# Kernel optimization log

Hardware: AMD Instinct MI355X
Metric: run time of the kernel (lower is better)

## Reference

```python
import jax, jax.numpy as jnp
import numpy as np

H_DIM = 512
FF_DIM = 2048
N_HEAD = 4
N_BLOCK = 3
N_TOKEN = 128
B, S = 8, 1024
LN_EPS = 1e-5


def _layernorm(x, g, b):
    mu = jnp.mean(x, axis=-1, keepdims=True)
    var = jnp.mean(jnp.square(x - mu), axis=-1, keepdims=True)
    return (x - mu) * jax.lax.rsqrt(var + LN_EPS) * g + b


def setup_inputs() -> dict:
    key = jax.random.key(0)
    ks = jax.random.split(key, 20)
    sc = 0.02
    inp = {
        'input_ids': jax.random.randint(ks[0], (B, S), 0, N_TOKEN, dtype=jnp.int32),
        'attention_mask': jnp.ones((B, S), dtype=jnp.int32),
        'emb': jax.random.uniform(ks[1], (N_TOKEN, H_DIM), dtype=jnp.float32),
        'wq': jax.random.normal(ks[2], (N_BLOCK, N_HEAD, H_DIM, H_DIM), dtype=jnp.float32) * sc,
        'wk': jax.random.normal(ks[3], (N_BLOCK, N_HEAD, H_DIM, H_DIM), dtype=jnp.float32) * sc,
        'wv': jax.random.normal(ks[4], (N_BLOCK, N_HEAD, H_DIM, H_DIM), dtype=jnp.float32) * sc,
        'wo_w': jax.random.normal(ks[5], (N_BLOCK, N_HEAD * H_DIM, H_DIM), dtype=jnp.float32) * sc,
        'wo_b': jnp.zeros((N_BLOCK, H_DIM), dtype=jnp.float32),
        'ln1_g': jnp.ones((N_BLOCK, H_DIM), dtype=jnp.float32),
        'ln1_b': jnp.zeros((N_BLOCK, H_DIM), dtype=jnp.float32),
        'ff1_w': jax.random.normal(ks[6], (N_BLOCK, FF_DIM, H_DIM), dtype=jnp.float32) * sc,
        'ff1_b': jnp.zeros((N_BLOCK, FF_DIM), dtype=jnp.float32),
        'ff2_w': jax.random.normal(ks[7], (N_BLOCK, H_DIM, FF_DIM), dtype=jnp.float32) * sc,
        'ff2_b': jnp.zeros((N_BLOCK, H_DIM), dtype=jnp.float32),
        'ln2_g': jnp.ones((N_BLOCK, H_DIM), dtype=jnp.float32),
        'ln2_b': jnp.zeros((N_BLOCK, H_DIM), dtype=jnp.float32),
        'lm_w': jax.random.normal(ks[8], (H_DIM, N_TOKEN), dtype=jnp.float32) * sc,
    }
    return inp


def reference(emb, wq, wk, wv, wo_w, wo_b, ln1_g, ln1_b, ff1_w, ff1_b,
              ff2_w, ff2_b, ln2_g, ln2_b, lm_w, input_ids, attention_mask):
    mask_f = attention_mask.astype(jnp.float32)          # [B,S]
    valid = attention_mask != 0                          # [B,S]

    # Embedding lookup
    x = emb[input_ids]                                   # [B,S,H]

    # Positional encoding: positions assigned sequentially to valid tokens;
    # both even and odd feature slots get the SAME sin value (per source).
    pos = jnp.cumsum(mask_f, axis=-1) - 1.0              # [B,S]
    div = jnp.exp(jnp.arange(0, H_DIM, 2, dtype=jnp.float32) * (-jnp.log(10000.0) / H_DIM))  # [H/2]
    s = jnp.sin(pos[..., None] * div)                    # [B,S,H/2]
    pos_enc = jnp.repeat(s, 2, axis=-1) * mask_f[..., None]
    x = x + pos_enc

    # Allowed attention: causal (key <= query) AND query valid AND key valid
    rows = jnp.arange(S)
    causal = rows[None, :, None] >= rows[None, None, :]  # [1,S,S] (query>=key)
    allowed = causal & valid[:, :, None] & valid[:, None, :]  # [B,S,S]
    neg_inf = jnp.float32(-jnp.inf)
    scale = jnp.sqrt(jnp.float32(H_DIM))

    for l in range(N_BLOCK):
        # Per-head full-width attention (each head uses full H_DIM)
        q = jnp.einsum('bsh,nhd->bnsd', x, wq[l])
        k = jnp.einsum('bsh,nhd->bnsd', x, wk[l])
        v = jnp.einsum('bsh,nhd->bnsd', x, wv[l])
        scores = jnp.einsum('bnsd,bntd->bnst', q, k) / scale      # [B,N,S,S]
        scores = jnp.where(allowed[:, None], scores, neg_inf)
        att = jax.nn.softmax(scores, axis=-1)
        att = jnp.where(jnp.isnan(att), 0.0, att)                  # NaN rows -> 0
        o = jnp.einsum('bnst,bntd->bnsd', att, v)                  # [B,N,S,H]
        o = jnp.transpose(o, (0, 2, 1, 3)).reshape(B, S, N_HEAD * H_DIM)
        mh = o @ wo_w[l] + wo_b[l]
        x = _layernorm(x + mh, ln1_g[l], ln1_b[l])
        # Conv1d with kernel 1 == pointwise linear
        ff = jax.nn.relu(jnp.einsum('bsh,fh->bsf', x, ff1_w[l]) + ff1_b[l])
        ff = jnp.einsum('bsf,hf->bsh', ff, ff2_w[l]) + ff2_b[l]
        x = _layernorm(x + ff, ln2_g[l], ln2_b[l])

    return x @ lm_w                                       # [B,S,N_TOKEN]
```

## Files before the change

kernel.cpp:

```cpp
#include <hip/hip_runtime.h>
#include <hip/hip_bf16.h>

#define S_LEN 1024
#define BATCH 8
#define HD 512
#define FFD 2048
#define NHEAD 4
#define NBLK 3
#define NTOK 128

typedef __bf16 bf16_t;
typedef __bf16 bf16x4_t __attribute__((ext_vector_type(4)));
typedef __bf16 bf16x8_t __attribute__((ext_vector_type(8)));
typedef float f32x4_t __attribute__((ext_vector_type(4)));

typedef __attribute__((address_space(3))) uint32_t lds_u32;
typedef __attribute__((address_space(1))) uint32_t glb_u32;

template<int NI>
__device__ __forceinline__ void ldsread(const bf16_t* __restrict__ buf, int row0,
                                        int fr, int fg, int sw, bf16x8_t (&dst)[NI][2]) {
  #pragma unroll
  for (int i = 0; i < NI; ++i)
    #pragma unroll
    for (int ks = 0; ks < 2; ++ks)
      dst[i][ks] = *(const bf16x8_t*)&buf[(row0 + i*16 + fr)*64 + (((ks*4 + fg) ^ sw) << 3)];
}

template<int IB, int JB>
__device__ __forceinline__ void mquad(f32x4_t (&acc)[8][4],
                                      const bf16x8_t (&af)[4][2], const bf16x8_t (&bf)[2][2]) {
  #pragma unroll
  for (int ks = 0; ks < 2; ++ks)
    #pragma unroll
    for (int i = 0; i < 4; ++i)
      #pragma unroll
      for (int j = 0; j < 2; ++j)
        acc[IB+i][JB+j] = __builtin_amdgcn_mfma_f32_16x16x32_bf16(af[i][ks], bf[j][ks], acc[IB+i][JB+j], 0, 0, 0);
}

template<bool OUT_BF16, bool BIAS, bool RELU, bool TRI, bool CKLIM, bool NORM>
__global__ __launch_bounds__(512, 2)
void gemm256_kernel(const bf16_t* __restrict__ A,
                    const bf16_t* __restrict__ Bt,
                    const float* __restrict__ bias,
                    void* __restrict__ Cv,
                    int M, int N, int K,
                    int lda, int ldb, int ldc,
                    long long sA, long long sB, int bshift, long long sBias,
                    int zshift, long long sC_hi, long long sC_lo,
                    int msub_shift, long long msub_stride,
                    float alpha)
{
  const int zb = blockIdx.z;
  int m0, n0;
  if (TRI) {
    const int idx = blockIdx.x;
    int mi = (int)((sqrtf(8.f * idx + 1.f) - 1.f) * 0.5f);
    while ((mi + 1) * (mi + 2) / 2 <= idx) ++mi;
    while (mi * (mi + 1) / 2 > idx) --mi;
    m0 = mi * 256;
    n0 = (idx - mi * (mi + 1) / 2) * 256;
  } else {
    m0 = blockIdx.x * 256;
    n0 = blockIdx.y * 256;
  }
  int kend = K;
  if (CKLIM) { int ke = m0 + 256; kend = ke < K ? ke : K; }
  const int nt = kend >> 6;

  const bf16_t* Az = A + (long long)zb * sA;
  const bf16_t* Bz = Bt + (long long)(zb >> bshift) * sB;
  const long long coff = ((long long)(zb >> zshift)) * sC_hi
                       + ((long long)(zb & ((1 << zshift) - 1))) * sC_lo;

  __shared__ __align__(16) bf16_t As[2][256 * 64];
  __shared__ __align__(16) bf16_t Bs[2][256 * 64];

  const int tid = threadIdx.x;
  const int lane = tid & 63;
  const int w = tid >> 6;
  const int wm = (w >> 2) * 128;
  const int wn = (w & 3) * 64;
  const int fr = lane & 15;
  const int fg = lane >> 4;
  const int sw = fr & 7;

  const int srow = tid >> 3;
  const int scol8 = tid & 7;
  const int gswz = ((scol8 ^ (srow & 7)) << 3);

  f32x4_t acc[8][4];
  #pragma unroll
  for (int i = 0; i < 8; ++i)
    #pragma unroll
    for (int j = 0; j < 4; ++j)
      acc[i][j] = (f32x4_t){0.f, 0.f, 0.f, 0.f};

  const bf16_t* gA0 = Az + (long long)(m0 + srow) * lda + gswz;
  const bf16_t* gB0 = Bz + (long long)(n0 + srow) * ldb + gswz;

  auto stage_half = [&](int buf, int kt, int h) {
    if (h < 2) {
      const bf16_t* g = gA0 + (long long)(h * 128) * lda + (kt << 6);
      bf16_t* l = &As[buf][(h*128 + srow) * 64 + (scol8 << 3)];
      __builtin_amdgcn_global_load_lds((const glb_u32*)g, (lds_u32*)l, 16, 0, 0);
      __builtin_amdgcn_global_load_lds((const glb_u32*)(g + 64LL*lda), (lds_u32*)(l + 64*64), 16, 0, 0);
    } else {
      const int hh = h - 2;
      const bf16_t* g = gB0 + (long long)(hh * 128) * ldb + (kt << 6);
      bf16_t* l = &Bs[buf][(hh*128 + srow) * 64 + (scol8 << 3)];
      __builtin_amdgcn_global_load_lds((const glb_u32*)g, (lds_u32*)l, 16, 0, 0);
      __builtin_amdgcn_global_load_lds((const glb_u32*)(g + 64LL*ldb), (lds_u32*)(l + 64*64), 16, 0, 0);
    }
  };

  stage_half(0, 0, 0); stage_half(0, 0, 1); stage_half(0, 0, 2); stage_half(0, 0, 3);
  if (nt > 1) { stage_half(1, 1, 0); stage_half(1, 1, 1); }
  if (nt > 1) asm volatile("s_waitcnt vmcnt(4)" ::: "memory");
  else        asm volatile("s_waitcnt vmcnt(0)" ::: "memory");
  __builtin_amdgcn_s_barrier();
  __builtin_amdgcn_sched_barrier(0);

  for (int t = 0; t < nt; ++t) {
    const int cur = t & 1;
    const bf16_t* Ac = &As[cur][0];
    const bf16_t* Bc = &Bs[cur][0];
    bf16x8_t a0[4][2], a1[4][2], b0[2][2], b1[2][2];

    ldsread<4>(Ac, wm, fr, fg, sw, a0);
    ldsread<2>(Bc, wn, fr, fg, sw, b0);
    if (t + 1 < nt) stage_half(cur ^ 1, t + 1, 2);
    mquad<0, 0>(acc, a0, b0);
    ldsread<4>(Ac, wm + 64, fr, fg, sw, a1);
    ldsread<2>(Bc, wn + 32, fr, fg, sw, b1);
    if (t + 1 < nt) stage_half(cur ^ 1, t + 1, 3);
    mquad<4, 2>(acc, a1, b1);

    __builtin_amdgcn_s_barrier();
    __builtin_amdgcn_sched_barrier(0);

    if (t + 2 < nt) stage_half(cur, t + 2, 0);
    mquad<0, 2>(acc, a0, b1);
    if (t + 2 < nt) {
      stage_half(cur, t + 2, 1);
      asm volatile("s_waitcnt vmcnt(4)" ::: "memory");
    } else {
      asm volatile("s_waitcnt vmcnt(0)" ::: "memory");
    }
    mquad<4, 0>(acc, a1, b0);

    __builtin_amdgcn_s_barrier();
    __builtin_amdgcn_sched_barrier(0);
  }

  #pragma unroll
  for (int i = 0; i < 8; ++i) {
    #pragma unroll
    for (int e = 0; e < 4; ++e) {
      const int row = m0 + wm + i*16 + fg*4 + e;
      const long long ro = coff
        + ((long long)(row >> msub_shift)) * msub_stride
        + (long long)(row & ((1 << msub_shift) - 1)) * (long long)ldc;
      float rn = 1.f;
      if (NORM) rn = bias[(long long)zb * sBias + row];
      #pragma unroll
      for (int j = 0; j < 4; ++j) {
        const int col = n0 + wn + j*16 + fr;
        float v = acc[i][j][e] * alpha;
        if (BIAS) v += bias[(long long)zb * sBias + col];
        if (NORM) v *= rn;
        if (RELU) v = v > 0.f ? v : 0.f;
        if (OUT_BF16) ((bf16_t*)Cv)[ro + col] = (bf16_t)v;
        else          ((float*)Cv)[ro + col]  = v;
      }
    }
  }
}

template<bool OUT_BF16, bool BIAS, bool RELU, bool CSKIP, bool CKLIM>
__global__ __launch_bounds__(256, 2)
void gemm_bt_kernel(const bf16_t* __restrict__ A,
                    const bf16_t* __restrict__ Bt,
                    const float* __restrict__ bias,
                    void* __restrict__ Cv,
                    int M, int N, int K,
                    int lda, int ldb, int ldc,
                    long long sA, long long sB, long long sBias,
                    int zshift, long long sC_hi, long long sC_lo,
                    int msub_shift, long long msub_stride,
                    float alpha)
{
  const int zb = blockIdx.z;
  const int m0 = blockIdx.x * 128;
  const int n0 = blockIdx.y * 128;
  if (CSKIP && n0 > m0 + 127) return;
  int kend = K;
  if (CKLIM) { int ke = m0 + 128; kend = ke < K ? ke : K; }

  const bf16_t* Az = A + (long long)zb * sA;
  const bf16_t* Bz = Bt + (long long)zb * sB;
  const long long coff = ((long long)(zb >> zshift)) * sC_hi
                       + ((long long)(zb & ((1 << zshift) - 1))) * sC_lo;

  __shared__ __align__(16) bf16_t As[128 * 64];
  __shared__ __align__(16) bf16_t Bs[128 * 64];

  const int tid = threadIdx.x;
  const int wv = tid >> 6;
  const int lane = tid & 63;
  const int wm = (wv >> 1) * 64;
  const int wn = (wv & 1) * 64;
  const int fr = lane & 15;
  const int fg = lane >> 4;
  const int sw = fr & 7;

  f32x4_t acc[4][4];
  #pragma unroll
  for (int i = 0; i < 4; ++i)
    #pragma unroll
    for (int j = 0; j < 4; ++j)
      acc[i][j] = (f32x4_t){0.f, 0.f, 0.f, 0.f};

  const bf16_t* ga = Az + (long long)(m0 + (wv << 5) + (lane >> 3)) * lda
                   + (((lane & 7) ^ (lane >> 3)) << 3);
  const bf16_t* gb = Bz + (long long)(n0 + (wv << 5) + (lane >> 3)) * ldb
                   + (((lane & 7) ^ (lane >> 3)) << 3);

  for (int k0 = 0; k0 < kend; k0 += 64) {
    #pragma unroll
    for (int s = 0; s < 4; ++s) {
      __builtin_amdgcn_global_load_lds(
        (const glb_u32*)(ga + (long long)s * 8 * lda + k0),
        (lds_u32*)(As + (wv * 4 + s) * 512), 16, 0, 0);
      __builtin_amdgcn_global_load_lds(
        (const glb_u32*)(gb + (long long)s * 8 * ldb + k0),
        (lds_u32*)(Bs + (wv * 4 + s) * 512), 16, 0, 0);
    }
    __syncthreads();
    #pragma unroll
    for (int kc = 0; kc < 2; ++kc) {
      const int ca = ((kc * 4 + fg) ^ sw) << 3;
      bf16x8_t af[4], bfr[4];
      #pragma unroll
      for (int i = 0; i < 4; ++i)
        af[i] = *(const bf16x8_t*)&As[(wm + i*16 + fr) * 64 + ca];
      #pragma unroll
      for (int j = 0; j < 4; ++j)
        bfr[j] = *(const bf16x8_t*)&Bs[(wn + j*16 + fr) * 64 + ca];
      #pragma unroll
      for (int i = 0; i < 4; ++i)
        #pragma unroll
        for (int j = 0; j < 4; ++j)
          acc[i][j] = __builtin_amdgcn_mfma_f32_16x16x32_bf16(af[i], bfr[j], acc[i][j], 0, 0, 0);
    }
    __syncthreads();
  }

  #pragma unroll
  for (int i = 0; i < 4; ++i) {
    #pragma unroll
    for (int e = 0; e < 4; ++e) {
      const int row = m0 + wm + i*16 + fg*4 + e;
      const long long ro = coff
        + ((long long)(row >> msub_shift)) * msub_stride
        + (long long)(row & ((1 << msub_shift) - 1)) * (long long)ldc;
      #pragma unroll
      for (int j = 0; j < 4; ++j) {
        const int col = n0 + wn + j*16 + fr;
        float v = acc[i][j][e] * alpha;
        if (BIAS) v += bias[(long long)zb * sBias + col];
        if (RELU) v = v > 0.f ? v : 0.f;
        if (OUT_BF16) ((bf16_t*)Cv)[ro + col] = (bf16_t)v;
        else          ((float*)Cv)[ro + col]  = v;
      }
    }
  }
}

__global__ void softmax_kernel(bf16_t* __restrict__ scP,
                               const int* __restrict__ mask, int pair0)
{
  const int lane = threadIdx.x & 63;
  const int s = blockIdx.x * 4 + (threadIdx.x >> 6);
  const int pz = blockIdx.y;
  const int b = (pair0 + pz) >> 2;
  bf16_t* row = scP + ((long long)pz * S_LEN + s) * S_LEN;
  const int t0 = lane * 16;

  bf16x8_t r0 = *(const bf16x8_t*)&row[t0];
  bf16x8_t r1 = *(const bf16x8_t*)&row[t0 + 8];
  int4 m4[4];
  #pragma unroll
  for (int q = 0; q < 4; ++q) m4[q] = *(const int4*)&mask[b * S_LEN + t0 + q*4];
  const int* mm = (const int*)m4;

  float v[16]; bool ok[16];
  #pragma unroll
  for (int j = 0; j < 16; ++j) {
    const int t = t0 + j;
    ok[j] = (t <= s) && (mm[j] != 0);
    float raw = (j < 8) ? (float)r0[j] : (float)r1[j - 8];
    v[j] = ok[j] ? raw : -INFINITY;
  }
  float mx = v[0];
  #pragma unroll
  for (int j = 1; j < 16; ++j) mx = fmaxf(mx, v[j]);
  #pragma unroll
  for (int o = 32; o; o >>= 1) mx = fmaxf(mx, __shfl_xor(mx, o));

  float e[16]; float sum = 0.f;
  #pragma unroll
  for (int j = 0; j < 16; ++j) { e[j] = ok[j] ? __expf(v[j] - mx) : 0.f; sum += e[j]; }
  #pragma unroll
  for (int o = 32; o; o >>= 1) sum += __shfl_xor(sum, o);

  const bool qvalid = mask[b * S_LEN + s] != 0;
  const float inv = (qvalid && sum > 0.f) ? 1.f / sum : 0.f;
  bf16x8_t o0, o1;
  #pragma unroll
  for (int j = 0; j < 8; ++j) { o0[j] = (bf16_t)(e[j] * inv); o1[j] = (bf16_t)(e[j+8] * inv); }
  *(bf16x8_t*)&row[t0] = o0;
  *(bf16x8_t*)&row[t0 + 8] = o1;
}

template<typename TIN>
__global__ void transpose_kernel(const TIN* __restrict__ in, bf16_t* __restrict__ out,
                                 int R, int C, long long sIn, long long sOut)
{
  __shared__ float tile[32][33];
  const long long zi = (long long)blockIdx.z * sIn;
  const long long zo = (long long)blockIdx.z * sOut;
  const int c0 = blockIdx.x * 32, r0 = blockIdx.y * 32;
  const int tx = threadIdx.x, ty = threadIdx.y;
  #pragma unroll
  for (int i = 0; i < 4; ++i) {
    int r = r0 + ty + i*8;
    tile[ty + i*8][tx] = (float)in[zi + (long long)r * C + c0 + tx];
  }
  __syncthreads();
  #pragma unroll
  for (int i = 0; i < 4; ++i) {
    int c = c0 + ty + i*8;
    out[zo + (long long)c * R + r0 + tx] = (bf16_t)tile[tx][ty + i*8];
  }
}

__global__ void convert2_kernel(const float* __restrict__ a, const float* __restrict__ b,
                                bf16_t* __restrict__ out, long long n)
{
  long long i = (long long)blockIdx.x * blockDim.x + threadIdx.x;
  long long stride = (long long)gridDim.x * blockDim.x;
  for (; i < 2*n; i += stride)
    out[i] = (bf16_t)(i < n ? a[i] : b[i - n]);
}

__global__ void fill_kernel(float* __restrict__ out, long long n, float v)
{
  long long i = (long long)blockIdx.x * blockDim.x + threadIdx.x;
  long long stride = (long long)gridDim.x * blockDim.x;
  for (; i < n; i += stride) out[i] = v;
}

__global__ void pos_kernel(const int* __restrict__ mask, float* __restrict__ pos)
{
  __shared__ float scn[S_LEN];
  const int b = blockIdx.x, t = threadIdx.x;
  scn[t] = (float)(mask[b * S_LEN + t] != 0);
  __syncthreads();
  for (int off = 1; off < S_LEN; off <<= 1) {
    float add = (t >= off) ? scn[t - off] : 0.f;
    __syncthreads();
    scn[t] += add;
    __syncthreads();
  }
  pos[b * S_LEN + t] = scn[t] - 1.0f;
}

__global__ void embed_kernel(const int* __restrict__ ids, const int* __restrict__ mask,
                             const float* __restrict__ pos, const float* __restrict__ emb,
                             float* __restrict__ x, bf16_t* __restrict__ xb)
{
  const int idx = blockIdx.x * 256 + threadIdx.x;
  const int i = idx & 255;
  const int bs = idx >> 8;
  const int id = ids[bs];
  const float m = (float)(mask[bs] != 0);
  const float p = pos[bs];
  const float dv = __expf(-(float)(2 * i) * (9.210340371976184f / (float)HD));
  const float sv = __sinf(p * dv) * m;
  const float e0 = emb[id * HD + 2*i], e1 = emb[id * HD + 2*i + 1];
  const float x0 = e0 + sv, x1 = e1 + sv;
  x[(long long)bs * HD + 2*i]     = x0;
  x[(long long)bs * HD + 2*i + 1] = x1;
  xb[(long long)bs * HD + 2*i]     = (bf16_t)x0;
  xb[(long long)bs * HD + 2*i + 1] = (bf16_t)x1;
}

__global__ void ln_kernel(float* __restrict__ x, const float* __restrict__ tparts,
                          int ns, long long pstride,
                          const float* __restrict__ bias,
                          const float* __restrict__ g, const float* __restrict__ b,
                          bf16_t* __restrict__ xb)
{
  const int lane = threadIdx.x & 63;
  const long long row = (long long)blockIdx.x * 4 + (threadIdx.x >> 6);
  const int e0 = lane * 8;
  const long long base = row * HD + e0;

  float4 xa = *(const float4*)&x[base];
  float4 xc = *(const float4*)&x[base + 4];
  float4 ba = *(const float4*)&bias[e0];
  float4 bc = *(const float4*)&bias[e0 + 4];
  float v[8] = {xa.x+ba.x, xa.y+ba.y, xa.z+ba.z, xa.w+ba.w,
                xc.x+bc.x, xc.y+bc.y, xc.z+bc.z, xc.w+bc.w};
  for (int i = 0; i < ns; ++i) {
    float4 p0 = *(const float4*)&tparts[i*pstride + base];
    float4 p1 = *(const float4*)&tparts[i*pstride + base + 4];
    v[0]+=p0.x; v[1]+=p0.y; v[2]+=p0.z; v[3]+=p0.w;
    v[4]+=p1.x; v[5]+=p1.y; v[6]+=p1.z; v[7]+=p1.w;
  }
  float s = 0.f;
  #pragma unroll
  for (int j = 0; j < 8; ++j) s += v[j];
  #pragma unroll
  for (int o = 32; o; o >>= 1) s += __shfl_xor(s, o);
  const float mu = s * (1.f / (float)HD);
  float q = 0.f;
  #pragma unroll
  for (int j = 0; j < 8; ++j) { v[j] -= mu; q += v[j]*v[j]; }
  #pragma unroll
  for (int o = 32; o; o >>= 1) q += __shfl_xor(q, o);
  const float inv = rsqrtf(q * (1.f / (float)HD) + 1e-5f);

  float4 ga4 = *(const float4*)&g[e0];
  float4 gc4 = *(const float4*)&g[e0 + 4];
  float4 bb4 = *(const float4*)&b[e0];
  float4 bd4 = *(const float4*)&b[e0 + 4];
  float y[8] = {v[0]*inv*ga4.x+bb4.x, v[1]*inv*ga4.y+bb4.y, v[2]*inv*ga4.z+bb4.z, v[3]*inv*ga4.w+bb4.w,
                v[4]*inv*gc4.x+bd4.x, v[5]*inv*gc4.y+bd4.y, v[6]*inv*gc4.z+bd4.z, v[7]*inv*gc4.w+bd4.w};
  *(float4*)&x[base]     = (float4){y[0],y[1],y[2],y[3]};
  *(float4*)&x[base + 4] = (float4){y[4],y[5],y[6],y[7]};
  bf16x8_t yb;
  #pragma unroll
  for (int j = 0; j < 8; ++j) yb[j] = (bf16_t)y[j];
  *(bf16x8_t*)&xb[base] = yb;
}

extern "C" void kernel_launch(void* const* d_in, const int* in_sizes, int n_in,
                              void* d_out, int out_size, void* d_ws, size_t ws_size,
                              hipStream_t stream)
{
  (void)in_sizes; (void)n_in;
  const int*   ids   = (const int*)d_in[0];
  const int*   amask = (const int*)d_in[1];
  const float* emb   = (const float*)d_in[2];
  const float* wq    = (const float*)d_in[3];
  const float* wk    = (const float*)d_in[4];
  const float* wv    = (const float*)d_in[5];
  const float* wo_w  = (const float*)d_in[6];
  const float* wo_b  = (const float*)d_in[7];
  const float* ln1_g = (const float*)d_in[8];
  const float* ln1_b = (const float*)d_in[9];
  const float* ff1_w = (const float*)d_in[10];
  const float* ff1_b = (const float*)d_in[11];
  const float* ff2_w = (const float*)d_in[12];
  const float* ff2_b = (const float*)d_in[13];
  const float* ln2_g = (const float*)d_in[14];
  const float* ln2_b = (const float*)d_in[15];
  const float* lm_w  = (const float*)d_in[16];

  const long long MROW = (long long)BATCH * S_LEN;
  const size_t MBc = 1ull << 20;
  char* p = (char*)d_ws;
  auto alloc = [&](size_t bytes) { char* r = p; p += (bytes + 255) & ~(size_t)255; return r; };

  float*  x     = (float*) alloc(MROW * HD * 4);
  bf16_t* xb    = (bf16_t*)alloc(MROW * HD * 2);
  bf16_t* ob    = (bf16_t*)alloc(MROW * (NHEAD*HD) * 2);
  bf16_t* wqkb  = (bf16_t*)alloc(8LL * HD * HD * 2);
  bf16_t* wvT   = (bf16_t*)alloc(4LL * HD * HD * 2);
  bf16_t* Gt    = (bf16_t*)alloc(4LL * HD * HD * 2);
  bf16_t* woT   = (bf16_t*)alloc((long long)HD * FFD * 2);
  bf16_t* wff1  = (bf16_t*)alloc((long long)FFD * HD * 2);
  bf16_t* wff2  = (bf16_t*)alloc((long long)HD * FFD * 2);
  bf16_t* lmT   = (bf16_t*)alloc((long long)NTOK * HD * 2);
  float*  pos   = (float*) alloc(MROW * 4);

  const size_t used = (size_t)(p - (char*)d_ws);
  const size_t rem  = ws_size > used ? ws_size - used : 0;

  int P = 0, SK = 2;
  if      (rem >= 128 * MBc) { P = 32; SK = 4; }
  else if (rem >= 64 * MBc)  { P = 8;  SK = 2; }
  if (P == 0) {
    fill_kernel<<<1024, 256, 0, stream>>>((float*)d_out, (long long)out_size,
                                          (float)(ws_size >> 20));
    return;
  }

  char* A = p;
  const long long pairE = (long long)S_LEN * HD;
  bf16_t* qc  = (bf16_t*)A;
  bf16_t* vTc = qc  + (long long)P * pairE;
  bf16_t* scb = vTc + (long long)P * pairE;
  float*  tmp = (float*)A;
  bf16_t* ffb = (bf16_t*)(A + (size_t)SK * 16 * MBc);

  const dim3 tb(32, 8);
  transpose_kernel<float><<<dim3(4,16,1), tb, 0, stream>>>(lm_w, lmT, HD, NTOK, 0, 0);
  pos_kernel<<<BATCH, S_LEN, 0, stream>>>(amask, pos);
  embed_kernel<<<8192, 256, 0, stream>>>(ids, amask, pos, emb, x, xb);

  const int nch = 32 / P;
  const int bpc = P / NHEAD;

  for (int l = 0; l < NBLK; ++l) {
    convert2_kernel<<<2048, 256, 0, stream>>>(
      wq + (long long)l*NHEAD*HD*HD, wk + (long long)l*NHEAD*HD*HD, wqkb, 4LL*HD*HD);
    transpose_kernel<float><<<dim3(16,16,4), tb, 0, stream>>>(
      wv + (long long)l*NHEAD*HD*HD, wvT, HD, HD, (long long)HD*HD, (long long)HD*HD);
    transpose_kernel<float><<<dim3(16,64,1), tb, 0, stream>>>(
      wo_w + (long long)l*FFD*HD, woT, FFD, HD, 0, 0);
    convert2_kernel<<<2048, 256, 0, stream>>>(
      ff1_w + (long long)l*FFD*HD, ff2_w + (long long)l*HD*FFD, wff1, (long long)FFD*HD);
    gemm_bt_kernel<true,false,false,false,false><<<dim3(4,4,4),256,0,stream>>>(
      wqkb + 4LL*HD*HD, wqkb, nullptr, Gt,
      HD, HD, HD, HD, HD, HD,
      (long long)HD*HD, (long long)HD*HD, 0,
      30, 0, (long long)HD*HD,
      30, 0, 1.f);

    for (int c = 0; c < nch; ++c) {
      const int b0 = c * bpc;
      const int pair0 = b0 * NHEAD;
      const int Mch = bpc * S_LEN;

      gemm256_kernel<true,false,false,false,false,false><<<dim3(Mch/256,2,4),512,0,stream>>>(
        xb + (long long)b0*S_LEN*HD, Gt, nullptr, qc, Mch, HD, HD, HD, HD, HD,
        0, (long long)HD*HD, 0, 0,
        2, 0, pairE,
        10, (long long)NHEAD*pairE, 1.f);

      gemm256_kernel<true,false,false,false,false,false><<<dim3(8,4,bpc),512,0,stream>>>(
        wvT, xb + (long long)b0*S_LEN*HD, nullptr, vTc,
        2048, S_LEN, HD, HD, HD, S_LEN,
        0, (long long)S_LEN*HD, 0, 0,
        0, (long long)NHEAD*HD*S_LEN, 0,
        9, (long long)HD*S_LEN, 1.f);

      gemm256_kernel<true,false,false,true,false,false><<<dim3(10,1,P),512,0,stream>>>(
        qc, xb + (long long)b0*S_LEN*HD, nullptr, scb,
        S_LEN, S_LEN, HD, HD, HD, S_LEN,
        pairE, (long long)S_LEN*HD, 2, 0,
        30, 0, (long long)S_LEN*S_LEN,
        30, 0, 0.044194173824159216f);
      softmax_kernel<<<dim3(S_LEN/4,P),256,0,stream>>>(scb, amask, pair0);
      gemm256_kernel<true,false,false,false,true,false><<<dim3(4,2,P),512,0,stream>>>(
        scb, vTc, nullptr,
        ob + (long long)b0*S_LEN*(NHEAD*HD),
        S_LEN, HD, S_LEN, S_LEN, S_LEN, NHEAD*HD,
        (long long)S_LEN*S_LEN, (long long)HD*S_LEN, 0, 0,
        2, (long long)S_LEN*NHEAD*HD, HD,
        30, 0, 1.f);
    }

    gemm256_kernel<false,false,false,false,false,false><<<dim3(32,2,SK),512,0,stream>>>(
      ob, woT, nullptr, tmp,
      (int)MROW, HD, (NHEAD*HD)/SK, NHEAD*HD, NHEAD*HD, HD,
      (NHEAD*HD)/SK, (NHEAD*HD)/SK, 0, 0,
      0, (long long)MROW*HD, 0,
      30, 0, 1.f);
    ln_kernel<<<2048,256,0,stream>>>(x, tmp, SK, (long long)MROW*HD,
                                     wo_b + l*HD, ln1_g + l*HD, ln1_b + l*HD, xb);

    gemm256_kernel<true,true,true,false,false,false><<<dim3(32,8,1),512,0,stream>>>(
      xb, wff1, ff1_b + l*FFD, ffb,
      (int)MROW, FFD, HD, HD, HD, FFD,
      0, 0, 0, 0, 30, 0, 0, 30, 0, 1.f);
    gemm256_kernel<false,false,false,false,false,false><<<dim3(32,2,SK),512,0,stream>>>(
      ffb, wff2, nullptr, tmp,
      (int)MROW, HD, FFD/SK, FFD, FFD, HD,
      FFD/SK, FFD/SK, 0, 0,
      0, (long long)MROW*HD, 0,
      30, 0, 1.f);
    ln_kernel<<<2048,256,0,stream>>>(x, tmp, SK, (long long)MROW*HD,
                                     ff2_b + l*HD, ln2_g + l*HD, ln2_b + l*HD, xb);
  }

  gemm_bt_kernel<false,false,false,false,false><<<dim3(64,1,1),256,0,stream>>>(
    xb, lmT, nullptr, (float*)d_out,
    (int)MROW, NTOK, HD, HD, HD, NTOK,
    0, 0, 0, 30, 0, 0, 30, 0, 1.f);
}
```

Measured before the change: 864.0 us.

## Fold output projection into value weights and drop the Wo GEMM

Precomputes U_h = Wv_h·Wo_h per head, so each head's attention output is already projected to H_DIM. Per-head outputs go into four separate bf16 planes, and a new LayerNorm kernel sums the four planes with the residual and bias. This removes the large M×2048×512 output-projection GEMM and its fp32 split-K partials. The cost is an extra small weight GEMM per layer, plus summing bf16-rounded per-head partials, which changes precision.

```diff
diff --git a/kernel.cpp b/kernel.cpp
--- a/kernel.cpp
+++ b/kernel.cpp
@@ -447,6 +447,56 @@
   *(bf16x8_t*)&xb[base] = yb;
 }
 
+__global__ void lnb_kernel(float* __restrict__ x, const bf16_t* __restrict__ tparts,
+                           long long pstride,
+                           const float* __restrict__ bias,
+                           const float* __restrict__ g, const float* __restrict__ b,
+                           bf16_t* __restrict__ xb)
+{
+  const int lane = threadIdx.x & 63;
+  const long long row = (long long)blockIdx.x * 4 + (threadIdx.x >> 6);
+  const int e0 = lane * 8;
+  const long long base = row * HD + e0;
+
+  float4 xa = *(const float4*)&x[base];
+  float4 xc = *(const float4*)&x[base + 4];
+  float4 ba = *(const float4*)&bias[e0];
+  float4 bc = *(const float4*)&bias[e0 + 4];
+  float v[8] = {xa.x+ba.x, xa.y+ba.y, xa.z+ba.z, xa.w+ba.w,
+                xc.x+bc.x, xc.y+bc.y, xc.z+bc.z, xc.w+bc.w};
+  #pragma unroll
+  for (int i = 0; i < 4; ++i) {
+    bf16x8_t pp = *(const bf16x8_t*)&tparts[i*pstride + base];
+    #pragma unroll
+    for (int j = 0; j < 8; ++j) v[j] += (float)pp[j];
+  }
+  float s = 0.f;
+  #pragma unroll
+  for (int j = 0; j < 8; ++j) s += v[j];
+  #pragma unroll
+  for (int o = 32; o; o >>= 1) s += __shfl_xor(s, o);
+  const float mu = s * (1.f / (float)HD);
+  float q = 0.f;
+  #pragma unroll
+  for (int j = 0; j < 8; ++j) { v[j] -= mu; q += v[j]*v[j]; }
+  #pragma unroll
+  for (int o = 32; o; o >>= 1) q += __shfl_xor(q, o);
+  const float inv = rsqrtf(q * (1.f / (float)HD) + 1e-5f);
+
+  float4 ga4 = *(const float4*)&g[e0];
+  float4 gc4 = *(const float4*)&g[e0 + 4];
+  float4 bb4 = *(const float4*)&b[e0];
+  float4 bd4 = *(const float4*)&b[e0 + 4];
+  float y[8] = {v[0]*inv*ga4.x+bb4.x, v[1]*inv*ga4.y+bb4.y, v[2]*inv*ga4.z+bb4.z, v[3]*inv*ga4.w+bb4.w,
+                v[4]*inv*gc4.x+bd4.x, v[5]*inv*gc4.y+bd4.y, v[6]*inv*gc4.z+bd4.z, v[7]*inv*gc4.w+bd4.w};
+  *(float4*)&x[base]     = (float4){y[0],y[1],y[2],y[3]};
+  *(float4*)&x[base + 4] = (float4){y[4],y[5],y[6],y[7]};
+  bf16x8_t yb;
+  #pragma unroll
+  for (int j = 0; j < 8; ++j) yb[j] = (bf16_t)y[j];
+  *(bf16x8_t*)&xb[base] = yb;
+}
+
 extern "C" void kernel_launch(void* const* d_in, const int* in_sizes, int n_in,
                               void* d_out, int out_size, void* d_ws, size_t ws_size,
                               hipStream_t stream)
@@ -477,10 +527,11 @@
 
   float*  x     = (float*) alloc(MROW * HD * 4);
   bf16_t* xb    = (bf16_t*)alloc(MROW * HD * 2);
-  bf16_t* ob    = (bf16_t*)alloc(MROW * (NHEAD*HD) * 2);
+  bf16_t* ob    = (bf16_t*)alloc(4LL * MROW * HD * 2);
   bf16_t* wqkb  = (bf16_t*)alloc(8LL * HD * HD * 2);
-  bf16_t* wvT   = (bf16_t*)alloc(4LL * HD * HD * 2);
+  bf16_t* wvb   = (bf16_t*)alloc(4LL * HD * HD * 2);
   bf16_t* Gt    = (bf16_t*)alloc(4LL * HD * HD * 2);
+  bf16_t* UT    = (bf16_t*)alloc(4LL * HD * HD * 2);
   bf16_t* woT   = (bf16_t*)alloc((long long)HD * FFD * 2);
   bf16_t* wff1  = (bf16_t*)alloc((long long)FFD * HD * 2);
   bf16_t* wff2  = (bf16_t*)alloc((long long)HD * FFD * 2);
@@ -502,8 +553,8 @@
   char* A = p;
   const long long pairE = (long long)S_LEN * HD;
   bf16_t* qc  = (bf16_t*)A;
-  bf16_t* vTc = qc  + (long long)P * pairE;
-  bf16_t* scb = vTc + (long long)P * pairE;
+  bf16_t* uTc = qc  + (long long)P * pairE;
+  bf16_t* scb = uTc + (long long)P * pairE;
   float*  tmp = (float*)A;
   bf16_t* ffb = (bf16_t*)(A + (size_t)SK * 16 * MBc);
 
@@ -518,8 +569,9 @@
   for (int l = 0; l < NBLK; ++l) {
     convert2_kernel<<<2048, 256, 0, stream>>>(
       wq + (long long)l*NHEAD*HD*HD, wk + (long long)l*NHEAD*HD*HD, wqkb, 4LL*HD*HD);
-    transpose_kernel<float><<<dim3(16,16,4), tb, 0, stream>>>(
-      wv + (long long)l*NHEAD*HD*HD, wvT, HD, HD, (long long)HD*HD, (long long)HD*HD);
+    convert2_kernel<<<2048, 256, 0, stream>>>(
+      wv + (long long)l*NHEAD*HD*HD, wv + (long long)l*NHEAD*HD*HD + 2LL*HD*HD,
+      wvb, 2LL*HD*HD);
     transpose_kernel<float><<<dim3(16,64,1), tb, 0, stream>>>(
       wo_w + (long long)l*FFD*HD, woT, FFD, HD, 0, 0);
     convert2_kernel<<<2048, 256, 0, stream>>>(
@@ -530,6 +582,12 @@
       (long long)HD*HD, (long long)HD*HD, 0,
       30, 0, (long long)HD*HD,
       30, 0, 1.f);
+    gemm_bt_kernel<true,false,false,false,false><<<dim3(4,4,4),256,0,stream>>>(
+      woT, wvb, nullptr, UT,
+      HD, HD, HD, FFD, HD, HD,
+      512, (long long)HD*HD, 0,
+      30, 0, (long long)HD*HD,
+      30, 0, 1.f);
 
     for (int c = 0; c < nch; ++c) {
       const int b0 = c * bpc;
@@ -543,7 +601,7 @@
         10, (long long)NHEAD*pairE, 1.f);
 
       gemm256_kernel<true,false,false,false,false,false><<<dim3(8,4,bpc),512,0,stream>>>(
-        wvT, xb + (long long)b0*S_LEN*HD, nullptr, vTc,
+        UT, xb + (long long)b0*S_LEN*HD, nullptr, uTc,
         2048, S_LEN, HD, HD, HD, S_LEN,
         0, (long long)S_LEN*HD, 0, 0,
         0, (long long)NHEAD*HD*S_LEN, 0,
@@ -557,22 +615,15 @@
         30, 0, 0.044194173824159216f);
       softmax_kernel<<<dim3(S_LEN/4,P),256,0,stream>>>(scb, amask, pair0);
       gemm256_kernel<true,false,false,false,true,false><<<dim3(4,2,P),512,0,stream>>>(
-        scb, vTc, nullptr,
-        ob + (long long)b0*S_LEN*(NHEAD*HD),
-        S_LEN, HD, S_LEN, S_LEN, S_LEN, NHEAD*HD,
+        scb, uTc, nullptr, ob,
+        S_LEN, HD, S_LEN, S_LEN, S_LEN, HD,
         (long long)S_LEN*S_LEN, (long long)HD*S_LEN, 0, 0,
-        2, (long long)S_LEN*NHEAD*HD, HD,
+        2, (long long)S_LEN*HD, (long long)MROW*HD,
         30, 0, 1.f);
     }
 
-    gemm256_kernel<false,false,false,false,false,false><<<dim3(32,2,SK),512,0,stream>>>(
-      ob, woT, nullptr, tmp,
-      (int)MROW, HD, (NHEAD*HD)/SK, NHEAD*HD, NHEAD*HD, HD,
-      (NHEAD*HD)/SK, (NHEAD*HD)/SK, 0, 0,
-      0, (long long)MROW*HD, 0,
-      30, 0, 1.f);
-    ln_kernel<<<2048,256,0,stream>>>(x, tmp, SK, (long long)MROW*HD,
-                                     wo_b + l*HD, ln1_g + l*HD, ln1_b + l*HD, xb);
+    lnb_kernel<<<2048,256,0,stream>>>(x, ob, (long long)MROW*HD,
+                                      wo_b + l*HD, ln1_g + l*HD, ln1_b + l*HD, xb);
 
     gemm256_kernel<true,true,true,false,false,false><<<dim3(32,8,1),512,0,stream>>>(
       xb, wff1, ff1_b + l*FFD, ffb,
```

New measurement: 813.7 us. -5.8%, faster.
